# Optimization experiments

Measured on AMD Instinct MI355X. Metric: run time of the kernel, lower is better.

The kernel has to match this reference:

```python
import jax, jax.numpy as jnp
import numpy as np

EPS = 1e-12  # matches torch F.normalize default eps


def setup_inputs() -> dict:
    key = jax.random.key(0)
    k_h, = jax.random.split(key, 1)
    B, S, D = 4, 4096, 2048
    h = jax.random.normal(k_h, (B, S, D), dtype=jnp.float32)
    alpha = jnp.asarray(2.0, dtype=jnp.float32)  # alpha_init
    beta = jnp.asarray(0.5, dtype=jnp.float32)   # beta_init
    return {"h": h, "alpha": alpha, "beta": beta}


def reference(h, alpha, beta):
    # --- concentration: mean pairwise cosine similarity (off-diagonal) ---
    # F.normalize(h, dim=-1): x / max(||x||_2, eps)
    norm = jnp.linalg.norm(h, axis=-1, keepdims=True)
    h_norm = h / jnp.maximum(norm, EPS)
    # sim: (B, S, S) via batched GEMM, same as torch.bmm
    sim = jnp.einsum('bid,bjd->bij', h_norm, h_norm)
    B, S, _ = sim.shape
    # mean over all off-diagonal entries across the whole batch
    diag_sum = jnp.einsum('bii->', sim)
    denom = jnp.asarray(B * S * (S - 1), dtype=sim.dtype)
    conc = (jnp.sum(sim) - diag_sum) / denom
    lambda_t = jax.nn.sigmoid(alpha * (conc - beta))
    return (lambda_t, conc)
```

## Files before the change

### kernel.cpp

```cpp
#include <hip/hip_runtime.h>
#include <math.h>

#define NBATCH 4
#define SROWS  4096
#define DCOLS  2048
#define BPB    128
#define NBLK1  (NBATCH * BPB)
#define ROWS_PER_WAVE (SROWS / (BPB * 4))

#define SSQ_OFFSET ((size_t)NBLK1 * DCOLS)

typedef float v4f __attribute__((ext_vector_type(4)));

__global__ __launch_bounds__(256, 2)
void row_normalize_sum(const float* __restrict__ h, float* __restrict__ part,
                       unsigned* __restrict__ counter) {
    if (blockIdx.x == 0 && threadIdx.x == 0) *counter = 0u;

    const int b    = blockIdx.x >> 7;
    const int blk  = blockIdx.x & (BPB - 1);
    const int wave = threadIdx.x >> 6;
    const int lane = threadIdx.x & 63;

    const float* hb = h + (size_t)b * SROWS * DCOLS;
    const int wid      = blk * 4 + wave;
    const int row_base = wid * ROWS_PER_WAVE;

    float acc[32];
#pragma unroll
    for (int i = 0; i < 32; ++i) acc[i] = 0.0f;

    for (int r = 0; r < ROWS_PER_WAVE; r += 2) {
        const v4f* p0 = (const v4f*)(hb + (size_t)(row_base + r)     * DCOLS) + lane;
        const v4f* p1 = (const v4f*)(hb + (size_t)(row_base + r + 1) * DCOLS) + lane;
        v4f v0[8], v1[8];
#pragma unroll
        for (int s = 0; s < 8; ++s) v0[s] = __builtin_nontemporal_load(p0 + s * 64);
#pragma unroll
        for (int s = 0; s < 8; ++s) v1[s] = __builtin_nontemporal_load(p1 + s * 64);

        float ss0 = 0.0f, ss1 = 0.0f;
#pragma unroll
        for (int s = 0; s < 8; ++s) {
#pragma unroll
            for (int j = 0; j < 4; ++j) {
                ss0 += v0[s][j] * v0[s][j];
                ss1 += v1[s][j] * v1[s][j];
            }
        }
#pragma unroll
        for (int m = 32; m >= 1; m >>= 1) {
            ss0 += __shfl_xor(ss0, m, 64);
            ss1 += __shfl_xor(ss1, m, 64);
        }
        const float inv0 = (float)(1.0 / fmax(sqrt((double)ss0), 1e-12));
        const float inv1 = (float)(1.0 / fmax(sqrt((double)ss1), 1e-12));
#pragma unroll
        for (int s = 0; s < 8; ++s) {
#pragma unroll
            for (int j = 0; j < 4; ++j) {
                acc[s * 4 + j] += v0[s][j] * inv0;
                acc[s * 4 + j] += v1[s][j] * inv1;
            }
        }
    }

    __shared__ float red[4][DCOLS];
#pragma unroll
    for (int s = 0; s < 8; ++s) {
        v4f v;
#pragma unroll
        for (int j = 0; j < 4; ++j) v[j] = acc[s * 4 + j];
        *(v4f*)&red[wave][s * 256 + lane * 4] = v;
    }
    __syncthreads();

    float* dst = part + (size_t)blockIdx.x * DCOLS;
#pragma unroll
    for (int k = 0; k < 8; ++k) {
        const int c = k * 256 + threadIdx.x;
        dst[c] = red[0][c] + red[1][c] + red[2][c] + red[3][c];
    }
}

__global__ __launch_bounds__(256, 4)
void reduce_partials_finalize(const float* __restrict__ part,
                              double* __restrict__ ssq_part,
                              unsigned* __restrict__ counter,
                              const float* __restrict__ alpha,
                              const float* __restrict__ beta,
                              float* __restrict__ out) {
    const int b    = blockIdx.x >> 4;
    const int c    = ((blockIdx.x & 15) * 128) + (threadIdx.x & 127);
    const int half = threadIdx.x >> 7;
    const float* pb = part + (size_t)b * BPB * DCOLS;

    double sum = 0.0;
    const int pstart = half * 64;
#pragma unroll 16
    for (int p = pstart; p < pstart + 64; ++p)
        sum += (double)pb[(size_t)p * DCOLS + c];

    __shared__ double sh[256];
    sh[threadIdx.x] = sum;
    __syncthreads();

    double ssq = 0.0;
    if (threadIdx.x < 128) {
        const double s2 = sh[threadIdx.x] + sh[threadIdx.x + 128];
        ssq = s2 * s2;
    }
    __syncthreads();
    sh[threadIdx.x] = ssq;
    __syncthreads();
    for (int off = 64; off > 0; off >>= 1) {
        if (threadIdx.x < off) sh[threadIdx.x] += sh[threadIdx.x + off];
        __syncthreads();
    }

    __shared__ int lastFlag;
    if (threadIdx.x == 0) {
        __hip_atomic_store(&ssq_part[blockIdx.x], sh[0],
                           __ATOMIC_RELEASE, __HIP_MEMORY_SCOPE_AGENT);
        const unsigned t = __hip_atomic_fetch_add(counter, 1u,
                           __ATOMIC_ACQ_REL, __HIP_MEMORY_SCOPE_AGENT);
        lastFlag = (t == 63u) ? 1 : 0;
    }
    __syncthreads();

    if (lastFlag && threadIdx.x < 64) {
        double v = __hip_atomic_load(&ssq_part[threadIdx.x],
                                     __ATOMIC_ACQUIRE, __HIP_MEMORY_SCOPE_AGENT);
#pragma unroll
        for (int m = 32; m >= 1; m >>= 1) v += __shfl_xor(v, m, 64);
        if (threadIdx.x == 0) {
            const double num   = v - (double)NBATCH * (double)SROWS;
            const double denom = (double)NBATCH * (double)SROWS * (double)(SROWS - 1);
            const double conc  = num / denom;
            const double a  = (double)alpha[0];
            const double bt = (double)beta[0];
            const double lam = 1.0 / (1.0 + exp(-a * (conc - bt)));
            out[0] = (float)lam;
            out[1] = (float)conc;
        }
    }
}

extern "C" void kernel_launch(void* const* d_in, const int* in_sizes, int n_in,
                              void* d_out, int out_size, void* d_ws, size_t ws_size,
                              hipStream_t stream) {
    (void)in_sizes; (void)n_in; (void)out_size; (void)ws_size;
    const float* h     = (const float*)d_in[0];
    const float* alpha = (const float*)d_in[1];
    const float* beta  = (const float*)d_in[2];
    float* out         = (float*)d_out;
    float* part        = (float*)d_ws;
    double* ssq_part   = (double*)((float*)d_ws + SSQ_OFFSET);
    unsigned* counter  = (unsigned*)(ssq_part + 64);

    row_normalize_sum<<<NBLK1, 256, 0, stream>>>(h, part, counter);
    reduce_partials_finalize<<<64, 256, 0, stream>>>(part, ssq_part, counter,
                                                     alpha, beta, out);
}
```

Before: 187.6 us.

## Fuse row-normalize and partial reduction into one cooperative kernel with grid sync

Merges the two kernels into a single cooperative launch that uses grid-wide syncs between the row-normalize/column-sum phase, the per-batch partial reduction, and the final scalar computation. This removes the second launch and the atomic counter/last-block pattern. In exchange, all 512 blocks must be co-resident, and two grid.sync barriers are added, each of which costs a global synchronisation.

```diff
diff --git a/kernel.cpp b/kernel.cpp
--- a/kernel.cpp
+++ b/kernel.cpp
@@ -1,5 +1,8 @@
 #include <hip/hip_runtime.h>
+#include <hip/hip_cooperative_groups.h>
 #include <math.h>
+
+namespace cg = cooperative_groups;
 
 #define NBATCH 4
 #define SROWS  4096
@@ -13,124 +16,117 @@
 typedef float v4f __attribute__((ext_vector_type(4)));
 
 __global__ __launch_bounds__(256, 2)
-void row_normalize_sum(const float* __restrict__ h, float* __restrict__ part,
-                       unsigned* __restrict__ counter) {
-    if (blockIdx.x == 0 && threadIdx.x == 0) *counter = 0u;
+void fused_all(const float* __restrict__ h, float* __restrict__ part,
+               double* __restrict__ ssq_part,
+               const float* __restrict__ alpha, const float* __restrict__ beta,
+               float* __restrict__ out) {
+    cg::grid_group grid = cg::this_grid();
+    __shared__ float red[4][DCOLS];
 
-    const int b    = blockIdx.x >> 7;
-    const int blk  = blockIdx.x & (BPB - 1);
-    const int wave = threadIdx.x >> 6;
-    const int lane = threadIdx.x & 63;
+    {
+        const int b    = blockIdx.x >> 7;
+        const int blk  = blockIdx.x & (BPB - 1);
+        const int wave = threadIdx.x >> 6;
+        const int lane = threadIdx.x & 63;
 
-    const float* hb = h + (size_t)b * SROWS * DCOLS;
-    const int wid      = blk * 4 + wave;
-    const int row_base = wid * ROWS_PER_WAVE;
+        const float* hb = h + (size_t)b * SROWS * DCOLS;
+        const int wid      = blk * 4 + wave;
+        const int row_base = wid * ROWS_PER_WAVE;
 
-    float acc[32];
+        float acc[32];
 #pragma unroll
-    for (int i = 0; i < 32; ++i) acc[i] = 0.0f;
+        for (int i = 0; i < 32; ++i) acc[i] = 0.0f;
 
-    for (int r = 0; r < ROWS_PER_WAVE; r += 2) {
-        const v4f* p0 = (const v4f*)(hb + (size_t)(row_base + r)     * DCOLS) + lane;
-        const v4f* p1 = (const v4f*)(hb + (size_t)(row_base + r + 1) * DCOLS) + lane;
-        v4f v0[8], v1[8];
+        for (int r = 0; r < ROWS_PER_WAVE; r += 2) {
+            const v4f* p0 = (const v4f*)(hb + (size_t)(row_base + r)     * DCOLS) + lane;
+            const v4f* p1 = (const v4f*)(hb + (size_t)(row_base + r + 1) * DCOLS) + lane;
+            v4f v0[8], v1[8];
 #pragma unroll
-        for (int s = 0; s < 8; ++s) v0[s] = __builtin_nontemporal_load(p0 + s * 64);
+            for (int s = 0; s < 8; ++s) v0[s] = __builtin_nontemporal_load(p0 + s * 64);
 #pragma unroll
-        for (int s = 0; s < 8; ++s) v1[s] = __builtin_nontemporal_load(p1 + s * 64);
+            for (int s = 0; s < 8; ++s) v1[s] = __builtin_nontemporal_load(p1 + s * 64);
 
-        float ss0 = 0.0f, ss1 = 0.0f;
+            float ss0 = 0.0f, ss1 = 0.0f;
+#pragma unroll
+            for (int s = 0; s < 8; ++s) {
+#pragma unroll
+                for (int j = 0; j < 4; ++j) {
+                    ss0 += v0[s][j] * v0[s][j];
+                    ss1 += v1[s][j] * v1[s][j];
+                }
+            }
+#pragma unroll
+            for (int m = 32; m >= 1; m >>= 1) {
+                ss0 += __shfl_xor(ss0, m, 64);
+                ss1 += __shfl_xor(ss1, m, 64);
+            }
+            const float inv0 = (float)(1.0 / fmax(sqrt((double)ss0), 1e-12));
+            const float inv1 = (float)(1.0 / fmax(sqrt((double)ss1), 1e-12));
+#pragma unroll
+            for (int s = 0; s < 8; ++s) {
+#pragma unroll
+                for (int j = 0; j < 4; ++j) {
+                    acc[s * 4 + j] += v0[s][j] * inv0;
+                    acc[s * 4 + j] += v1[s][j] * inv1;
+                }
+            }
+        }
+
 #pragma unroll
         for (int s = 0; s < 8; ++s) {
+            v4f v;
 #pragma unroll
-            for (int j = 0; j < 4; ++j) {
-                ss0 += v0[s][j] * v0[s][j];
-                ss1 += v1[s][j] * v1[s][j];
-            }
+            for (int j = 0; j < 4; ++j) v[j] = acc[s * 4 + j];
+            *(v4f*)&red[wave][s * 256 + lane * 4] = v;
         }
+        __syncthreads();
+
+        float* dst = part + (size_t)blockIdx.x * DCOLS;
 #pragma unroll
-        for (int m = 32; m >= 1; m >>= 1) {
-            ss0 += __shfl_xor(ss0, m, 64);
-            ss1 += __shfl_xor(ss1, m, 64);
-        }
-        const float inv0 = (float)(1.0 / fmax(sqrt((double)ss0), 1e-12));
-        const float inv1 = (float)(1.0 / fmax(sqrt((double)ss1), 1e-12));
-#pragma unroll
-        for (int s = 0; s < 8; ++s) {
-#pragma unroll
-            for (int j = 0; j < 4; ++j) {
-                acc[s * 4 + j] += v0[s][j] * inv0;
-                acc[s * 4 + j] += v1[s][j] * inv1;
-            }
+        for (int k = 0; k < 8; ++k) {
+            const int c = k * 256 + threadIdx.x;
+            dst[c] = red[0][c] + red[1][c] + red[2][c] + red[3][c];
         }
     }
 
-    __shared__ float red[4][DCOLS];
-#pragma unroll
-    for (int s = 0; s < 8; ++s) {
-        v4f v;
-#pragma unroll
-        for (int j = 0; j < 4; ++j) v[j] = acc[s * 4 + j];
-        *(v4f*)&red[wave][s * 256 + lane * 4] = v;
-    }
-    __syncthreads();
+    grid.sync();
 
-    float* dst = part + (size_t)blockIdx.x * DCOLS;
-#pragma unroll
-    for (int k = 0; k < 8; ++k) {
-        const int c = k * 256 + threadIdx.x;
-        dst[c] = red[0][c] + red[1][c] + red[2][c] + red[3][c];
-    }
-}
+    if (blockIdx.x < 64) {
+        const int k    = blockIdx.x;
+        const int b    = k >> 4;
+        const int c    = ((k & 15) * 128) + (threadIdx.x & 127);
+        const int half = threadIdx.x >> 7;
+        const float* pb = part + (size_t)b * BPB * DCOLS;
 
-__global__ __launch_bounds__(256, 4)
-void reduce_partials_finalize(const float* __restrict__ part,
-                              double* __restrict__ ssq_part,
-                              unsigned* __restrict__ counter,
-                              const float* __restrict__ alpha,
-                              const float* __restrict__ beta,
-                              float* __restrict__ out) {
-    const int b    = blockIdx.x >> 4;
-    const int c    = ((blockIdx.x & 15) * 128) + (threadIdx.x & 127);
-    const int half = threadIdx.x >> 7;
-    const float* pb = part + (size_t)b * BPB * DCOLS;
+        double sum = 0.0;
+        const int pstart = half * 64;
+#pragma unroll 16
+        for (int p = pstart; p < pstart + 64; ++p)
+            sum += (double)pb[(size_t)p * DCOLS + c];
 
-    double sum = 0.0;
-    const int pstart = half * 64;
-#pragma unroll 16
-    for (int p = pstart; p < pstart + 64; ++p)
-        sum += (double)pb[(size_t)p * DCOLS + c];
+        double* sh = (double*)&red[0][0];
+        sh[threadIdx.x] = sum;
+        __syncthreads();
 
-    __shared__ double sh[256];
-    sh[threadIdx.x] = sum;
-    __syncthreads();
-
-    double ssq = 0.0;
-    if (threadIdx.x < 128) {
-        const double s2 = sh[threadIdx.x] + sh[threadIdx.x + 128];
-        ssq = s2 * s2;
-    }
-    __syncthreads();
-    sh[threadIdx.x] = ssq;
-    __syncthreads();
-    for (int off = 64; off > 0; off >>= 1) {
-        if (threadIdx.x < off) sh[threadIdx.x] += sh[threadIdx.x + off];
+        double ssq = 0.0;
+        if (threadIdx.x < 128) {
+            const double s2 = sh[threadIdx.x] + sh[threadIdx.x + 128];
+            ssq = s2 * s2;
+        }
         __syncthreads();
+        sh[threadIdx.x] = ssq;
+        __syncthreads();
+        for (int off = 64; off > 0; off >>= 1) {
+            if (threadIdx.x < off) sh[threadIdx.x] += sh[threadIdx.x + off];
+            __syncthreads();
+        }
+        if (threadIdx.x == 0) ssq_part[k] = sh[0];
     }
 
-    __shared__ int lastFlag;
-    if (threadIdx.x == 0) {
-        __hip_atomic_store(&ssq_part[blockIdx.x], sh[0],
-                           __ATOMIC_RELEASE, __HIP_MEMORY_SCOPE_AGENT);
-        const unsigned t = __hip_atomic_fetch_add(counter, 1u,
-                           __ATOMIC_ACQ_REL, __HIP_MEMORY_SCOPE_AGENT);
-        lastFlag = (t == 63u) ? 1 : 0;
-    }
-    __syncthreads();
+    grid.sync();
 
-    if (lastFlag && threadIdx.x < 64) {
-        double v = __hip_atomic_load(&ssq_part[threadIdx.x],
-                                     __ATOMIC_ACQUIRE, __HIP_MEMORY_SCOPE_AGENT);
+    if (blockIdx.x == 0 && threadIdx.x < 64) {
+        double v = ssq_part[threadIdx.x];
 #pragma unroll
         for (int m = 32; m >= 1; m >>= 1) v += __shfl_xor(v, m, 64);
         if (threadIdx.x == 0) {
@@ -156,9 +152,9 @@
     float* out         = (float*)d_out;
     float* part        = (float*)d_ws;
     double* ssq_part   = (double*)((float*)d_ws + SSQ_OFFSET);
-    unsigned* counter  = (unsigned*)(ssq_part + 64);
 
-    row_normalize_sum<<<NBLK1, 256, 0, stream>>>(h, part, counter);
-    reduce_partials_finalize<<<64, 256, 0, stream>>>(part, ssq_part, counter,
-                                                     alpha, beta, out);
+    void* args[] = { (void*)&h, (void*)&part, (void*)&ssq_part,
+                     (void*)&alpha, (void*)&beta, (void*)&out };
+    hipLaunchCooperativeKernel((void*)fused_all, dim3(NBLK1), dim3(256),
+                               args, 0, stream);
 }
```

Measured after the change: 301.3 us. +60.6%, slower.
